# Kernel optimization log

Hardware: AMD Instinct MI355X
Metric: run time of the kernel (lower is better)

Reference implementation:

```python
import jax, jax.numpy as jnp
import numpy as np

# attn_reps = "8x0n+30x1n": per head channel C = 8 scalars + 30 Lorentz four-vectors (4 each) = 128
N_SCALARS, N_VECTORS = 8, 30
ETA = jnp.diag(jnp.array([1.0, -1.0, -1.0, -1.0], dtype=jnp.float32))  # Minkowski metric


def _quat_to_rot(q):
    # q: (M,4) unit quaternions -> (M,3,3) rotation matrices
    w, x, y, z = q[:, 0], q[:, 1], q[:, 2], q[:, 3]
    r0 = jnp.stack([1 - 2 * (y * y + z * z), 2 * (x * y - w * z), 2 * (x * z + w * y)], axis=-1)
    r1 = jnp.stack([2 * (x * y + w * z), 1 - 2 * (x * x + z * z), 2 * (y * z - w * x)], axis=-1)
    r2 = jnp.stack([2 * (x * z - w * y), 2 * (y * z + w * x), 1 - 2 * (x * x + y * y)], axis=-1)
    return jnp.stack([r0, r1, r2], axis=-2)


def _random_lorentz(key, M):
    # random proper Lorentz transforms: boost(beta) @ blockdiag(1, R)
    k1, k2 = jax.random.split(key)
    quat = jax.random.normal(k1, (M, 4), dtype=jnp.float32)
    quat = quat / jnp.linalg.norm(quat, axis=-1, keepdims=True)
    R = _quat_to_rot(quat)  # (M,3,3)
    beta = jax.random.uniform(k2, (M, 3), minval=-1.0, maxval=1.0, dtype=jnp.float32) * (0.6 / np.sqrt(3.0))
    b2 = jnp.sum(beta * beta, axis=-1)  # (M,), < 0.36
    gamma = 1.0 / jnp.sqrt(1.0 - b2)
    n = beta / jnp.sqrt(jnp.maximum(b2, 1e-12))[:, None]
    gb = gamma[:, None] * beta  # (M,3)
    top = jnp.concatenate([gamma[:, None], gb], axis=-1)[:, None, :]  # (M,1,4)
    spatial = jnp.eye(3, dtype=jnp.float32) + (gamma - 1.0)[:, None, None] * n[:, :, None] * n[:, None, :]
    bottom = jnp.concatenate([gb[:, :, None], spatial], axis=-1)  # (M,3,4)
    B = jnp.concatenate([top, bottom], axis=-2)  # (M,4,4) boost
    rot4 = jnp.zeros((M, 4, 4), dtype=jnp.float32).at[:, 0, 0].set(1.0).at[:, 1:, 1:].set(R)
    return jnp.einsum('mij,mjk->mik', B, rot4)


def setup_inputs() -> dict:
    key = jax.random.key(0)
    kq, kk, kv, kl = jax.random.split(key, 4)
    B, H, N, C = 8, 8, 1024, 128
    q = jax.random.normal(kq, (B, H, N, C), dtype=jnp.float32)
    k = jax.random.normal(kk, (B, H, N, C), dtype=jnp.float32)
    v = jax.random.normal(kv, (B, H, N, C), dtype=jnp.float32)
    L = _random_lorentz(kl, B * N).reshape(B, N, 4, 4)
    return {"q_local": q, "k_local": k, "v_local": v, "lframes_matrices": L}


def _transform(x, M):
    # TensorRepsTransform: scalars pass through, four-vectors get v' = M v (per particle)
    # x: (B,H,N,C), M: (B,N,4,4)
    s = x[..., :N_SCALARS]
    vec = x[..., N_SCALARS:].reshape(x.shape[:-1] + (N_VECTORS, 4))
    vec = jnp.einsum('bnij,bhnvj->bhnvi', M, vec)
    return jnp.concatenate([s, vec.reshape(x.shape[:-1] + (N_VECTORS * 4,))], axis=-1)


def reference(q_local, k_local, v_local, lframes_matrices):
    C = q_local.shape[-1]
    # InverseLFrames: Lorentz inverse  Lambda^{-1} = eta Lambda^T eta
    inv = jnp.einsum('ij,bnkj,kl->bnil', ETA, lframes_matrices, ETA)
    # LowerIndices: lower the output index -> eta @ Lambda^{-1}
    lower_inv = jnp.einsum('ij,bnjk->bnik', ETA, inv)
    q_g = _transform(q_local, inv)
    k_g = _transform(k_local, lower_inv)
    v_g = _transform(v_local, inv)
    # standard SDPA (scale 1/sqrt(C))
    scores = jnp.einsum('bhqc,bhkc->bhqk', q_g, k_g) * (1.0 / np.sqrt(C))
    attn = jax.nn.softmax(scores, axis=-1)
    out_g = jnp.einsum('bhqk,bhkc->bhqc', attn, v_g)
    # back to local frame with Lambda itself
    return _transform(out_g, lframes_matrices)
```

## Files before the change

### kernel.cpp

```cpp
#include <hip/hip_runtime.h>
#include <math.h>

typedef _Float16 f16;
typedef _Float16 f16x4 __attribute__((ext_vector_type(4)));
typedef _Float16 f16x8 __attribute__((ext_vector_type(8)));
typedef float    f32x4 __attribute__((ext_vector_type(4)));

typedef const __attribute__((address_space(1))) void gv_t;
typedef __attribute__((address_space(3))) void lv_t;

#define NSEQ 1024
#define CD   128
#define LT   136


__global__ __launch_bounds__(256)
void ipa_pre(const float* __restrict__ kg, const float* __restrict__ vg,
             const float* __restrict__ Lm, f16* __restrict__ khs, f16* __restrict__ vhs)
{
    __shared__ float LL[64 * 16];
    __shared__ __align__(16) f16 Kt[64 * LT];
    __shared__ __align__(16) f16 Vt[64 * LT];
    const int bx = blockIdx.x, nt = blockIdx.y, tid = threadIdx.x;
    const int bh = ((bx & 7) << 3) | (bx >> 3);
    const int b  = bh >> 3;
    const float* Lb = Lm + ((size_t)b * NSEQ + nt * 64) * 16;
    for (int t = tid; t < 64 * 16; t += 256) LL[t] = Lb[t];
    __syncthreads();

    const size_t base = ((size_t)bh * NSEQ + nt * 64) * CD;
    #pragma unroll
    for (int it = 0; it < 8; ++it) {
        int g = it * 256 + tid;
        int row = g >> 5, cg = g & 31;
        size_t idx = base + row * CD + cg * 4;
        const float* Lr = &LL[row * 16];
        float4 xk = *(const float4*)(kg + idx);
        float4 xv = *(const float4*)(vg + idx);
        float4 yk = xk, yv = xv;
        if (cg >= 2) {
            float t0 = xk.x, t1 = -xk.y, t2 = -xk.z, t3 = -xk.w;
            yk.x = Lr[0]*t0 + Lr[4]*t1 + Lr[8] *t2 + Lr[12]*t3;
            yk.y = Lr[1]*t0 + Lr[5]*t1 + Lr[9] *t2 + Lr[13]*t3;
            yk.z = Lr[2]*t0 + Lr[6]*t1 + Lr[10]*t2 + Lr[14]*t3;
            yk.w = Lr[3]*t0 + Lr[7]*t1 + Lr[11]*t2 + Lr[15]*t3;
            t0 = xv.x; t1 = -xv.y; t2 = -xv.z; t3 = -xv.w;
            yv.x =  (Lr[0]*t0 + Lr[4]*t1 + Lr[8] *t2 + Lr[12]*t3);
            yv.y = -(Lr[1]*t0 + Lr[5]*t1 + Lr[9] *t2 + Lr[13]*t3);
            yv.z = -(Lr[2]*t0 + Lr[6]*t1 + Lr[10]*t2 + Lr[14]*t3);
            yv.w = -(Lr[3]*t0 + Lr[7]*t1 + Lr[11]*t2 + Lr[15]*t3);
        }
        f16x4 hk = {(f16)yk.x, (f16)yk.y, (f16)yk.z, (f16)yk.w};
        f16x4 hv = {(f16)yv.x, (f16)yv.y, (f16)yv.z, (f16)yv.w};
        *(f16x4*)&Kt[row * LT + cg * 4] = hk;
        *(f16x4*)&Vt[row * LT + cg * 4] = hv;
    }
    __syncthreads();

    f16* kout = khs + (size_t)bh * 131072 + (size_t)nt * 4 * 4 * 512;
    #pragma unroll
    for (int it = 0; it < 4; ++it) {
        int slot = it * 256 + tid;
        int g16l = slot >> 8, cs = (slot >> 6) & 3, L = slot & 63;
        int lq = L & 15, quad = L >> 4;
        int keyl = ((g16l >> 1) << 5) + ((lq >> 2) << 3) + ((g16l & 1) << 2) + (lq & 3);
        f16x8 kv = *(const f16x8*)&Kt[keyl * LT + cs * 32 + quad * 8];
        *(f16x8*)(kout + (g16l * 4 + cs) * 512 + L * 8) = kv;
    }
    f16* vout = vhs + (size_t)bh * 131072 + (size_t)nt * 2 * 8 * 512;
    #pragma unroll
    for (int it = 0; it < 4; ++it) {
        int slot = it * 256 + tid;
        int k32l = slot >> 9, cb = (slot >> 6) & 7, L = slot & 63;
        int lq = L & 15, quad = L >> 4;
        int c = cb * 16 + lq;
        f16x8 o;
        #pragma unroll
        for (int j = 0; j < 8; ++j)
            o[j] = Vt[(k32l * 32 + quad * 8 + j) * LT + c];
        *(f16x8*)(vout + (k32l * 8 + cb) * 512 + L * 8) = o;
    }
}

__global__ __launch_bounds__(256, 2)
void ipa_attn(const float* __restrict__ qg, const f16* __restrict__ khs,
              const f16* __restrict__ vhs, const float* __restrict__ Lm,
              float* __restrict__ out)
{
    __shared__ __align__(16) f16 sK[2][4096];
    __shared__ __align__(16) f16 sV[2][4096];
    const int n = blockIdx.x;
    const int bh = ((n & 7) << 3) | ((n >> 3) & 7);
    const int b  = bh >> 3;
    const int tid = threadIdx.x;
    const int w = tid >> 6, lane = tid & 63, lq = lane & 15, quad = lane >> 4;
    const int qblk = n >> 6;
    const int q0 = qblk * 64 + w * 16;
    const f16* kbh = khs + (size_t)bh * 131072;
    const f16* vbh = vhs + (size_t)bh * 131072;
    const float sc2 = 0.12751744154226873f;

    auto stage = [&](int nb, int it) {
        const char* kp = (const char*)(kbh + (size_t)it * 4096);
        const char* vp = (const char*)(vbh + (size_t)it * 4096);
        char* kd = (char*)&sK[nb][0];
        char* vd = (char*)&sV[nb][0];
        #pragma unroll
        for (int j = 0; j < 2; ++j) {
            int off = (w * 2 + j) * 1024;
            __builtin_amdgcn_global_load_lds((gv_t*)(kp + off + lane * 16),
                                             (lv_t*)(kd + off), 16, 0, 0);
            __builtin_amdgcn_global_load_lds((gv_t*)(vp + off + lane * 16),
                                             (lv_t*)(vd + off), 16, 0, 0);
        }
    };

    f16x8 qf[4];
    {
        int qrow = q0 + lq;
        const float* Lr = Lm + ((size_t)b * NSEQ + qrow) * 16;
        const float* qp = qg + ((size_t)bh * NSEQ + qrow) * CD;
        float Lv[16];
        #pragma unroll
        for (int i = 0; i < 4; ++i) *(float4*)&Lv[i*4] = *(const float4*)(Lr + i*4);
        #pragma unroll
        for (int cs = 0; cs < 4; ++cs) {
            int c0 = cs * 32 + quad * 8;
            float4 x0 = *(const float4*)(qp + c0);
            float4 x1 = *(const float4*)(qp + c0 + 4);
            if (c0 >= 8) {
                float t0 = x0.x, t1 = -x0.y, t2 = -x0.z, t3 = -x0.w;
                float4 y;
                y.x =  (Lv[0]*t0 + Lv[4]*t1 + Lv[8] *t2 + Lv[12]*t3);
                y.y = -(Lv[1]*t0 + Lv[5]*t1 + Lv[9] *t2 + Lv[13]*t3);
                y.z = -(Lv[2]*t0 + Lv[6]*t1 + Lv[10]*t2 + Lv[14]*t3);
                y.w = -(Lv[3]*t0 + Lv[7]*t1 + Lv[11]*t2 + Lv[15]*t3);
                x0 = y;
                t0 = x1.x; t1 = -x1.y; t2 = -x1.z; t3 = -x1.w;
                y.x =  (Lv[0]*t0 + Lv[4]*t1 + Lv[8] *t2 + Lv[12]*t3);
                y.y = -(Lv[1]*t0 + Lv[5]*t1 + Lv[9] *t2 + Lv[13]*t3);
                y.z = -(Lv[2]*t0 + Lv[6]*t1 + Lv[10]*t2 + Lv[14]*t3);
                y.w = -(Lv[3]*t0 + Lv[7]*t1 + Lv[11]*t2 + Lv[15]*t3);
                x1 = y;
            }
            qf[cs] = (f16x8){(f16)(x0.x*sc2), (f16)(x0.y*sc2), (f16)(x0.z*sc2), (f16)(x0.w*sc2),
                             (f16)(x1.x*sc2), (f16)(x1.y*sc2), (f16)(x1.z*sc2), (f16)(x1.w*sc2)};
        }
    }

    f32x4 oacc[8];
    #pragma unroll
    for (int cb = 0; cb < 8; ++cb) oacc[cb] = (f32x4){0.f, 0.f, 0.f, 0.f};
    float mrun = -1e30f, lrun = 0.f;

    stage(0, 0);

    for (int it = 0; it < 32; ++it) {
        const int cur = it & 1;
        __syncthreads();
        if (it < 31) stage(cur ^ 1, it + 1);

        const f16* kb = &sK[cur][0];
        const f16* vb = &sV[cur][0];

        f32x4 s[2];
        s[0] = (f32x4){0.f, 0.f, 0.f, 0.f};
        s[1] = (f32x4){0.f, 0.f, 0.f, 0.f};
        #pragma unroll
        for (int cs = 0; cs < 4; ++cs) {
            f16x8 kf0 = *(const f16x8*)&kb[(cs    ) * 512 + lane * 8];
            f16x8 kf1 = *(const f16x8*)&kb[(cs + 4) * 512 + lane * 8];
            s[0] = __builtin_amdgcn_mfma_f32_16x16x32_f16(kf0, qf[cs], s[0], 0, 0, 0);
            s[1] = __builtin_amdgcn_mfma_f32_16x16x32_f16(kf1, qf[cs], s[1], 0, 0, 0);
        }

        float mx = fmaxf(fmaxf(fmaxf(s[0].x, s[0].y), fmaxf(s[0].z, s[0].w)),
                         fmaxf(fmaxf(s[1].x, s[1].y), fmaxf(s[1].z, s[1].w)));
        mx = fmaxf(mx, __shfl_xor(mx, 16, 64));
        mx = fmaxf(mx, __shfl_xor(mx, 32, 64));
        float mnew = fmaxf(mrun, mx);
        if (!__all(mx <= mrun)) {
            float alpha = exp2f(mrun - mnew);
            lrun *= alpha;
            #pragma unroll
            for (int cb = 0; cb < 8; ++cb) oacc[cb] *= alpha;
            mrun = mnew;
        }
        float p[8];
        p[0] = exp2f(s[0].x - mnew); p[1] = exp2f(s[0].y - mnew);
        p[2] = exp2f(s[0].z - mnew); p[3] = exp2f(s[0].w - mnew);
        p[4] = exp2f(s[1].x - mnew); p[5] = exp2f(s[1].y - mnew);
        p[6] = exp2f(s[1].z - mnew); p[7] = exp2f(s[1].w - mnew);
        lrun += ((p[0]+p[1]) + (p[2]+p[3])) + ((p[4]+p[5]) + (p[6]+p[7]));
        f16x8 pf = {(f16)p[0],(f16)p[1],(f16)p[2],(f16)p[3],
                    (f16)p[4],(f16)p[5],(f16)p[6],(f16)p[7]};

        #pragma unroll
        for (int cb = 0; cb < 8; ++cb) {
            f16x8 vf = *(const f16x8*)&vb[cb * 512 + lane * 8];
            oacc[cb] = __builtin_amdgcn_mfma_f32_16x16x32_f16(vf, pf, oacc[cb], 0, 0, 0);
        }
    }

    {
        float l = lrun;
        l += __shfl_xor(l, 16, 64);
        l += __shfl_xor(l, 32, 64);
        float invl = 1.0f / l;
        int qrow = q0 + lq;
        const float* Lr = Lm + ((size_t)b * NSEQ + qrow) * 16;
        float* ob = out + ((size_t)bh * NSEQ + qrow) * CD;
        #pragma unroll
        for (int cb = 0; cb < 8; ++cb) {
            int c0 = cb * 16 + quad * 4;
            float o0 = oacc[cb].x*invl, o1 = oacc[cb].y*invl;
            float o2 = oacc[cb].z*invl, o3 = oacc[cb].w*invl;
            float4 r;
            if (c0 >= 8) {
                r.x = Lr[0] *o0 + Lr[1] *o1 + Lr[2] *o2 + Lr[3] *o3;
                r.y = Lr[4] *o0 + Lr[5] *o1 + Lr[6] *o2 + Lr[7] *o3;
                r.z = Lr[8] *o0 + Lr[9] *o1 + Lr[10]*o2 + Lr[11]*o3;
                r.w = Lr[12]*o0 + Lr[13]*o1 + Lr[14]*o2 + Lr[15]*o3;
            } else {
                r.x = o0; r.y = o1; r.z = o2; r.w = o3;
            }
            *(float4*)(ob + c0) = r;
        }
    }
}

extern "C" void kernel_launch(void* const* d_in, const int* in_sizes, int n_in,
                              void* d_out, int out_size, void* d_ws, size_t ws_size,
                              hipStream_t stream) {
    const float* q = (const float*)d_in[0];
    const float* k = (const float*)d_in[1];
    const float* v = (const float*)d_in[2];
    const float* L = (const float*)d_in[3];
    float* o = (float*)d_out;
    f16* khs = (f16*)d_ws;
    f16* vhs = khs + (size_t)64 * 131072;
    dim3 grid1(64, 16);
    ipa_pre<<<grid1, 256, 0, stream>>>(k, v, L, khs, vhs);
    ipa_attn<<<1024, 256, 0, stream>>>(q, khs, vhs, L, o);
}
```

Measured before the change: 196.5 us.

## Switch attention to 32x32 MFMA tiles with 32 queries per wave

Each wave now computes 32 query rows using 32x32x16 f16 MFMAs instead of 16 rows with 16x16x32, so each block covers 128 queries and the grid halves. The pre-kernel rewrites K/V into the matching fragment layout, and probabilities are exchanged between half-waves with shuffles to form the PV operand. The aim is to double reuse of each staged K/V tile and use the larger MFMA shape. In exchange there are fewer blocks for parallelism, more accumulator registers and extra shuffle work.

```diff
diff --git a/kernel.cpp b/kernel.cpp
--- a/kernel.cpp
+++ b/kernel.cpp
@@ -2,9 +2,11 @@
 #include <math.h>
 
 typedef _Float16 f16;
+typedef _Float16 f16x2 __attribute__((ext_vector_type(2)));
 typedef _Float16 f16x4 __attribute__((ext_vector_type(4)));
 typedef _Float16 f16x8 __attribute__((ext_vector_type(8)));
 typedef float    f32x4 __attribute__((ext_vector_type(4)));
+typedef float    f32x16 __attribute__((ext_vector_type(16)));
 
 typedef const __attribute__((address_space(1))) void gv_t;
 typedef __attribute__((address_space(3))) void lv_t;
@@ -57,29 +59,32 @@
     }
     __syncthreads();
 
-    f16* kout = khs + (size_t)bh * 131072 + (size_t)nt * 4 * 4 * 512;
+    f16* kout = khs + (size_t)bh * 131072 + (size_t)(nt * 2) * 4096;
     #pragma unroll
     for (int it = 0; it < 4; ++it) {
         int slot = it * 256 + tid;
-        int g16l = slot >> 8, cs = (slot >> 6) & 3, L = slot & 63;
-        int lq = L & 15, quad = L >> 4;
-        int keyl = ((g16l >> 1) << 5) + ((lq >> 2) << 3) + ((g16l & 1) << 2) + (lq & 3);
-        f16x8 kv = *(const f16x8*)&Kt[keyl * LT + cs * 32 + quad * 8];
-        *(f16x8*)(kout + (g16l * 4 + cs) * 512 + L * 8) = kv;
-    }
-    f16* vout = vhs + (size_t)bh * 131072 + (size_t)nt * 2 * 8 * 512;
+        int kt2 = slot >> 9, cs16 = (slot >> 6) & 7, L = slot & 63;
+        int lq5 = L & 31, h = L >> 5;
+        f16x8 kv = *(const f16x8*)&Kt[(kt2 * 32 + lq5) * LT + cs16 * 16 + 8 * h];
+        *(f16x8*)(kout + (size_t)kt2 * 4096 + cs16 * 512 + L * 8) = kv;
+    }
+    f16* vout = vhs + (size_t)bh * 131072 + (size_t)(nt * 2) * 4096;
     #pragma unroll
     for (int it = 0; it < 4; ++it) {
         int slot = it * 256 + tid;
-        int k32l = slot >> 9, cb = (slot >> 6) & 7, L = slot & 63;
-        int lq = L & 15, quad = L >> 4;
-        int c = cb * 16 + lq;
+        int kt2 = slot >> 9, cb = (slot >> 7) & 3, kh = (slot >> 6) & 1, L = slot & 63;
+        int lq5 = L & 31, h = L >> 5;
+        int c = cb * 32 + lq5;
         f16x8 o;
         #pragma unroll
         for (int j = 0; j < 8; ++j)
-            o[j] = Vt[(k32l * 32 + quad * 8 + j) * LT + c];
-        *(f16x8*)(vout + (k32l * 8 + cb) * 512 + L * 8) = o;
-    }
+            o[j] = Vt[(kt2 * 32 + kh * 16 + 8 * h + j) * LT + c];
+        *(f16x8*)(vout + (size_t)kt2 * 4096 + (cb * 2 + kh) * 512 + L * 8) = o;
+    }
+}
+
+static __device__ __forceinline__ unsigned pk2(f16 a, f16 b) {
+    union { f16x2 h; unsigned u; } x; x.h = (f16x2){a, b}; return x.u;
 }
 
 __global__ __launch_bounds__(256, 2)
@@ -93,9 +98,10 @@
     const int bh = ((n & 7) << 3) | ((n >> 3) & 7);
     const int b  = bh >> 3;
     const int tid = threadIdx.x;
-    const int w = tid >> 6, lane = tid & 63, lq = lane & 15, quad = lane >> 4;
+    const int w = tid >> 6, lane = tid & 63;
+    const int lq5 = lane & 31, hh = lane >> 5;
     const int qblk = n >> 6;
-    const int q0 = qblk * 64 + w * 16;
+    const int q0 = qblk * 128 + w * 32;
     const f16* kbh = khs + (size_t)bh * 131072;
     const f16* vbh = vhs + (size_t)bh * 131072;
     const float sc2 = 0.12751744154226873f;
@@ -115,17 +121,17 @@
         }
     };
 
-    f16x8 qf[4];
+    f16x8 qf[8];
     {
-        int qrow = q0 + lq;
+        int qrow = q0 + lq5;
         const float* Lr = Lm + ((size_t)b * NSEQ + qrow) * 16;
         const float* qp = qg + ((size_t)bh * NSEQ + qrow) * CD;
         float Lv[16];
         #pragma unroll
         for (int i = 0; i < 4; ++i) *(float4*)&Lv[i*4] = *(const float4*)(Lr + i*4);
         #pragma unroll
-        for (int cs = 0; cs < 4; ++cs) {
-            int c0 = cs * 32 + quad * 8;
+        for (int cs = 0; cs < 8; ++cs) {
+            int c0 = cs * 16 + 8 * hh;
             float4 x0 = *(const float4*)(qp + c0);
             float4 x1 = *(const float4*)(qp + c0 + 4);
             if (c0 >= 8) {
@@ -148,9 +154,11 @@
         }
     }
 
-    f32x4 oacc[8];
-    #pragma unroll
-    for (int cb = 0; cb < 8; ++cb) oacc[cb] = (f32x4){0.f, 0.f, 0.f, 0.f};
+    f32x16 oacc[4];
+    #pragma unroll
+    for (int cb = 0; cb < 4; ++cb)
+        #pragma unroll
+        for (int r = 0; r < 16; ++r) oacc[cb][r] = 0.f;
     float mrun = -1e30f, lrun = 0.f;
 
     stage(0, 0);
@@ -163,68 +171,90 @@
         const f16* kb = &sK[cur][0];
         const f16* vb = &sV[cur][0];
 
-        f32x4 s[2];
-        s[0] = (f32x4){0.f, 0.f, 0.f, 0.f};
-        s[1] = (f32x4){0.f, 0.f, 0.f, 0.f};
-        #pragma unroll
-        for (int cs = 0; cs < 4; ++cs) {
-            f16x8 kf0 = *(const f16x8*)&kb[(cs    ) * 512 + lane * 8];
-            f16x8 kf1 = *(const f16x8*)&kb[(cs + 4) * 512 + lane * 8];
-            s[0] = __builtin_amdgcn_mfma_f32_16x16x32_f16(kf0, qf[cs], s[0], 0, 0, 0);
-            s[1] = __builtin_amdgcn_mfma_f32_16x16x32_f16(kf1, qf[cs], s[1], 0, 0, 0);
-        }
-
-        float mx = fmaxf(fmaxf(fmaxf(s[0].x, s[0].y), fmaxf(s[0].z, s[0].w)),
-                         fmaxf(fmaxf(s[1].x, s[1].y), fmaxf(s[1].z, s[1].w)));
-        mx = fmaxf(mx, __shfl_xor(mx, 16, 64));
+        f32x16 s;
+        #pragma unroll
+        for (int r = 0; r < 16; ++r) s[r] = 0.f;
+        #pragma unroll
+        for (int cs = 0; cs < 8; ++cs) {
+            f16x8 kf = *(const f16x8*)&kb[cs * 512 + lane * 8];
+            s = __builtin_amdgcn_mfma_f32_32x32x16_f16(kf, qf[cs], s, 0, 0, 0);
+        }
+
+        float mx = fmaxf(s[0], s[1]);
+        #pragma unroll
+        for (int r = 2; r < 16; ++r) mx = fmaxf(mx, s[r]);
         mx = fmaxf(mx, __shfl_xor(mx, 32, 64));
         float mnew = fmaxf(mrun, mx);
         if (!__all(mx <= mrun)) {
             float alpha = exp2f(mrun - mnew);
             lrun *= alpha;
             #pragma unroll
-            for (int cb = 0; cb < 8; ++cb) oacc[cb] *= alpha;
+            for (int cb = 0; cb < 4; ++cb) oacc[cb] *= alpha;
             mrun = mnew;
         }
-        float p[8];
-        p[0] = exp2f(s[0].x - mnew); p[1] = exp2f(s[0].y - mnew);
-        p[2] = exp2f(s[0].z - mnew); p[3] = exp2f(s[0].w - mnew);
-        p[4] = exp2f(s[1].x - mnew); p[5] = exp2f(s[1].y - mnew);
-        p[6] = exp2f(s[1].z - mnew); p[7] = exp2f(s[1].w - mnew);
-        lrun += ((p[0]+p[1]) + (p[2]+p[3])) + ((p[4]+p[5]) + (p[6]+p[7]));
-        f16x8 pf = {(f16)p[0],(f16)p[1],(f16)p[2],(f16)p[3],
-                    (f16)p[4],(f16)p[5],(f16)p[6],(f16)p[7]};
-
-        #pragma unroll
-        for (int cb = 0; cb < 8; ++cb) {
-            f16x8 vf = *(const f16x8*)&vb[cb * 512 + lane * 8];
-            oacc[cb] = __builtin_amdgcn_mfma_f32_16x16x32_f16(vf, pf, oacc[cb], 0, 0, 0);
-        }
+        float pr[16];
+        f16 ph[16];
+        #pragma unroll
+        for (int r = 0; r < 16; ++r) { pr[r] = exp2f(s[r] - mnew); ph[r] = (f16)pr[r]; }
+        float rs = ((pr[0]+pr[1])+(pr[2]+pr[3])) + ((pr[4]+pr[5])+(pr[6]+pr[7]))
+                 + ((pr[8]+pr[9])+(pr[10]+pr[11])) + ((pr[12]+pr[13])+(pr[14]+pr[15]));
+        lrun += rs;
+
+        f16x8 pf[2];
+        #pragma unroll
+        for (int kh = 0; kh < 2; ++kh) {
+            unsigned wA0 = pk2(ph[8*kh+0], ph[8*kh+1]);
+            unsigned wA1 = pk2(ph[8*kh+2], ph[8*kh+3]);
+            unsigned wB0 = pk2(ph[8*kh+4], ph[8*kh+5]);
+            unsigned wB1 = pk2(ph[8*kh+6], ph[8*kh+7]);
+            unsigned send0 = hh ? wA0 : wB0;
+            unsigned send1 = hh ? wA1 : wB1;
+            unsigned recv0 = __shfl_xor(send0, 32, 64);
+            unsigned recv1 = __shfl_xor(send1, 32, 64);
+            union { unsigned u[4]; f16x8 h; } pw;
+            pw.u[0] = hh ? recv0 : wA0;
+            pw.u[1] = hh ? recv1 : wA1;
+            pw.u[2] = hh ? wB0 : recv0;
+            pw.u[3] = hh ? wB1 : recv1;
+            pf[kh] = pw.h;
+        }
+
+        #pragma unroll
+        for (int cb = 0; cb < 4; ++cb)
+            #pragma unroll
+            for (int kh = 0; kh < 2; ++kh) {
+                f16x8 vf = *(const f16x8*)&vb[(cb * 2 + kh) * 512 + lane * 8];
+                oacc[cb] = __builtin_amdgcn_mfma_f32_32x32x16_f16(vf, pf[kh], oacc[cb], 0, 0, 0);
+            }
     }
 
     {
-        float l = lrun;
-        l += __shfl_xor(l, 16, 64);
-        l += __shfl_xor(l, 32, 64);
+        float l = lrun + __shfl_xor(lrun, 32, 64);
         float invl = 1.0f / l;
-        int qrow = q0 + lq;
+        int qrow = q0 + lq5;
         const float* Lr = Lm + ((size_t)b * NSEQ + qrow) * 16;
+        float Lv[16];
+        #pragma unroll
+        for (int i = 0; i < 4; ++i) *(float4*)&Lv[i*4] = *(const float4*)(Lr + i*4);
         float* ob = out + ((size_t)bh * NSEQ + qrow) * CD;
         #pragma unroll
-        for (int cb = 0; cb < 8; ++cb) {
-            int c0 = cb * 16 + quad * 4;
-            float o0 = oacc[cb].x*invl, o1 = oacc[cb].y*invl;
-            float o2 = oacc[cb].z*invl, o3 = oacc[cb].w*invl;
-            float4 r;
-            if (c0 >= 8) {
-                r.x = Lr[0] *o0 + Lr[1] *o1 + Lr[2] *o2 + Lr[3] *o3;
-                r.y = Lr[4] *o0 + Lr[5] *o1 + Lr[6] *o2 + Lr[7] *o3;
-                r.z = Lr[8] *o0 + Lr[9] *o1 + Lr[10]*o2 + Lr[11]*o3;
-                r.w = Lr[12]*o0 + Lr[13]*o1 + Lr[14]*o2 + Lr[15]*o3;
-            } else {
-                r.x = o0; r.y = o1; r.z = o2; r.w = o3;
+        for (int cb = 0; cb < 4; ++cb) {
+            #pragma unroll
+            for (int rg = 0; rg < 4; ++rg) {
+                int c0 = cb * 32 + rg * 8 + 4 * hh;
+                float o0 = oacc[cb][rg*4+0] * invl, o1 = oacc[cb][rg*4+1] * invl;
+                float o2 = oacc[cb][rg*4+2] * invl, o3 = oacc[cb][rg*4+3] * invl;
+                float4 r;
+                if (c0 >= 8) {
+                    r.x = Lv[0] *o0 + Lv[1] *o1 + Lv[2] *o2 + Lv[3] *o3;
+                    r.y = Lv[4] *o0 + Lv[5] *o1 + Lv[6] *o2 + Lv[7] *o3;
+                    r.z = Lv[8] *o0 + Lv[9] *o1 + Lv[10]*o2 + Lv[11]*o3;
+                    r.w = Lv[12]*o0 + Lv[13]*o1 + Lv[14]*o2 + Lv[15]*o3;
+                } else {
+                    r.x = o0; r.y = o1; r.z = o2; r.w = o3;
+                }
+                *(float4*)(ob + c0) = r;
             }
-            *(float4*)(ob + c0) = r;
         }
     }
 }
@@ -241,5 +271,5 @@
     f16* vhs = khs + (size_t)64 * 131072;
     dim3 grid1(64, 16);
     ipa_pre<<<grid1, 256, 0, stream>>>(k, v, L, khs, vhs);
-    ipa_attn<<<1024, 256, 0, stream>>>(q, khs, vhs, L, o);
-}
+    ipa_attn<<<512, 256, 0, stream>>>(q, khs, vhs, L, o);
+}
```

After: 197.6 us. No clear change (+0.6%).
